# Kernel tuning notes

Hardware: AMD Instinct MI355X
Metric: run time of the kernel (lower is better)

The kernel has to match this reference:

```python
import jax, jax.numpy as jnp
import numpy as np

VOCAB, DIM, HID, OUT = 400000, 300, 32, 2
BATCH, SEQ = 16384, 50

def setup_inputs() -> dict:
    key = jax.random.key(0)
    k_tok, k_emb, k_vw, k_vb, k_ww, k_wb = jax.random.split(key, 6)
    tokens = jax.random.randint(k_tok, (BATCH, SEQ), 0, VOCAB, dtype=jnp.int32)
    emb = jax.random.normal(k_emb, (VOCAB, DIM), dtype=jnp.float32) * 0.02
    emb = emb.at[0].set(0.0)  # padding_idx=0 row conventionally zero
    V_w = jax.random.normal(k_vw, (HID, DIM), dtype=jnp.float32) * (1.0 / np.sqrt(DIM))
    V_b = jnp.zeros((HID,), dtype=jnp.float32)
    W_w = jax.random.normal(k_ww, (OUT, HID), dtype=jnp.float32) * (1.0 / np.sqrt(HID))
    W_b = jnp.zeros((OUT,), dtype=jnp.float32)
    return {"tokens": tokens, "emb": emb, "V_w": V_w, "V_b": V_b, "W_w": W_w, "W_b": W_b}

def reference(tokens, emb, V_w, V_b, W_w, W_b):
    # gather [B,S,D] then mean-pool over words -> [B,D] (DAN average)
    pooled = jnp.mean(emb[tokens], axis=1)
    h = jax.nn.relu(pooled @ V_w.T + V_b)          # [B,HID]
    logits = h @ W_w.T + W_b                        # [B,OUT]
    # original module uses LogSoftmax(dim=0): normalize over the batch axis
    return jax.nn.log_softmax(logits, axis=0)
```

## Files before the change

### kernel.cpp

```cpp
#include <hip/hip_runtime.h>

#define VOCAB 400000
#define DIM   300
#define HID   32
#define NOUT  2
#define BATCH 16384
#define SEQ   50

__global__ __launch_bounds__(256) void dan_main(
    const int*   __restrict__ tokens,
    const float* __restrict__ emb,
    const float* __restrict__ Vw,
    const float* __restrict__ Vb,
    const float* __restrict__ Ww,
    const float* __restrict__ Wb,
    float*       __restrict__ logits)
{
    const int wave = threadIdx.x >> 6;
    const int lane = threadIdx.x & 63;
    const int row  = blockIdx.x * 4 + wave;
    if (row >= BATCH) return;

    const int* toks = tokens + row * SEQ;

    const bool has1 = (lane < (DIM / 4 - 64));

    float4 acc0 = make_float4(0.f, 0.f, 0.f, 0.f);
    float4 acc1 = make_float4(0.f, 0.f, 0.f, 0.f);

    for (int s = 0; s < SEQ; ++s) {
        const int t = toks[s];
        const float4* e = (const float4*)(emb + (size_t)t * DIM);
        float4 v0 = e[lane];
        acc0.x += v0.x; acc0.y += v0.y; acc0.z += v0.z; acc0.w += v0.w;
        if (has1) {
            float4 v1 = e[64 + lane];
            acc1.x += v1.x; acc1.y += v1.y; acc1.z += v1.z; acc1.w += v1.w;
        }
    }
    const float inv = 1.0f / (float)SEQ;
    acc0.x *= inv; acc0.y *= inv; acc0.z *= inv; acc0.w *= inv;
    acc1.x *= inv; acc1.y *= inv; acc1.z *= inv; acc1.w *= inv;

    float hp[HID];
    #pragma unroll
    for (int k = 0; k < HID; ++k) {
        const float4* vr = (const float4*)(Vw + k * DIM);
        float4 w0 = vr[lane];
        float p = acc0.x * w0.x + acc0.y * w0.y + acc0.z * w0.z + acc0.w * w0.w;
        if (has1) {
            float4 w1 = vr[64 + lane];
            p += acc1.x * w1.x + acc1.y * w1.y + acc1.z * w1.z + acc1.w * w1.w;
        }
        hp[k] = p;
    }

    #pragma unroll
    for (int m = 1; m < 64; m <<= 1) {
        #pragma unroll
        for (int k = 0; k < HID; ++k)
            hp[k] += __shfl_xor(hp[k], m, 64);
    }

    float l0 = Wb[0], l1 = Wb[1];
    #pragma unroll
    for (int k = 0; k < HID; ++k) {
        float h = hp[k] + Vb[k];
        h = h > 0.f ? h : 0.f;
        l0 += h * Ww[k];
        l1 += h * Ww[HID + k];
    }
    if (lane == 0) {
        logits[row * 2 + 0] = l0;
        logits[row * 2 + 1] = l1;
    }
}

__global__ __launch_bounds__(1024) void dan_reduce(
    const float* __restrict__ logits, float* __restrict__ c)
{
    __shared__ float r0[1024];
    __shared__ float r1[1024];
    const int tid = threadIdx.x;

    float m0 = -INFINITY, m1 = -INFINITY;
    for (int b = tid; b < BATCH; b += 1024) {
        m0 = fmaxf(m0, logits[b * 2 + 0]);
        m1 = fmaxf(m1, logits[b * 2 + 1]);
    }
    r0[tid] = m0; r1[tid] = m1;
    __syncthreads();
    for (int s = 512; s > 0; s >>= 1) {
        if (tid < s) {
            r0[tid] = fmaxf(r0[tid], r0[tid + s]);
            r1[tid] = fmaxf(r1[tid], r1[tid + s]);
        }
        __syncthreads();
    }
    m0 = r0[0]; m1 = r1[0];
    __syncthreads();

    float s0 = 0.f, s1 = 0.f;
    for (int b = tid; b < BATCH; b += 1024) {
        s0 += __expf(logits[b * 2 + 0] - m0);
        s1 += __expf(logits[b * 2 + 1] - m1);
    }
    r0[tid] = s0; r1[tid] = s1;
    __syncthreads();
    for (int s = 512; s > 0; s >>= 1) {
        if (tid < s) {
            r0[tid] += r0[tid + s];
            r1[tid] += r1[tid + s];
        }
        __syncthreads();
    }
    if (tid == 0) {
        c[0] = m0 + __logf(r0[0]);
        c[1] = m1 + __logf(r1[0]);
    }
}

__global__ __launch_bounds__(256) void dan_final(
    const float* __restrict__ logits, const float* __restrict__ c,
    float* __restrict__ out)
{
    const int idx = blockIdx.x * blockDim.x + threadIdx.x;
    if (idx < BATCH * NOUT)
        out[idx] = logits[idx] - c[idx & 1];
}

extern "C" void kernel_launch(void* const* d_in, const int* in_sizes, int n_in,
                              void* d_out, int out_size, void* d_ws, size_t ws_size,
                              hipStream_t stream) {
    const int*   tokens = (const int*)  d_in[0];
    const float* emb    = (const float*)d_in[1];
    const float* Vw     = (const float*)d_in[2];
    const float* Vb     = (const float*)d_in[3];
    const float* Ww     = (const float*)d_in[4];
    const float* Wb     = (const float*)d_in[5];
    float* out    = (float*)d_out;
    float* logits = (float*)d_ws;
    float* c      = logits + BATCH * NOUT;

    dan_main  <<<BATCH / 4, 256, 0, stream>>>(tokens, emb, Vw, Vb, Ww, Wb, logits);
    dan_reduce<<<1, 1024, 0, stream>>>(logits, c);
    dan_final <<<(BATCH * NOUT + 255) / 256, 256, 0, stream>>>(logits, c, out);
}
```

Baseline: 770.3 us.

## Restructure hidden projection via shared memory and fuse final normalization kernel

The pooled vector is staged in shared memory, and each lane then computes one hidden unit's half dot product, replacing the 32-entry per-lane register array and its 6-stage shuffle reduction over 32 values. The launch bounds now request 8 blocks per CU and the gather loop is unrolled to raise occupancy and memory-level parallelism for the embedding gather. The final log-softmax subtraction is folded into the single-block reduce kernel, which removes one launch but makes one block write all outputs. Each lane now reads Vw rows directly from global or L2 memory at row-strided addresses, and a block-wide barrier is added.

```diff
diff --git a/kernel.cpp b/kernel.cpp
--- a/kernel.cpp
+++ b/kernel.cpp
@@ -7,7 +7,7 @@
 #define BATCH 16384
 #define SEQ   50
 
-__global__ __launch_bounds__(256) void dan_main(
+__global__ __launch_bounds__(256, 8) void dan_main(
     const int*   __restrict__ tokens,
     const float* __restrict__ emb,
     const float* __restrict__ Vw,
@@ -19,15 +19,14 @@
     const int wave = threadIdx.x >> 6;
     const int lane = threadIdx.x & 63;
     const int row  = blockIdx.x * 4 + wave;
-    if (row >= BATCH) return;
 
     const int* toks = tokens + row * SEQ;
-
     const bool has1 = (lane < (DIM / 4 - 64));
 
     float4 acc0 = make_float4(0.f, 0.f, 0.f, 0.f);
     float4 acc1 = make_float4(0.f, 0.f, 0.f, 0.f);
 
+    #pragma unroll 5
     for (int s = 0; s < SEQ; ++s) {
         const int t = toks[s];
         const float4* e = (const float4*)(emb + (size_t)t * DIM);
@@ -40,44 +39,51 @@
     }
     const float inv = 1.0f / (float)SEQ;
     acc0.x *= inv; acc0.y *= inv; acc0.z *= inv; acc0.w *= inv;
-    acc1.x *= inv; acc1.y *= inv; acc1.z *= inv; acc1.w *= inv;
 
-    float hp[HID];
+    __shared__ float pool[4][304];
+    *(float4*)&pool[wave][4 * lane] = acc0;
+    if (has1) {
+        acc1.x *= inv; acc1.y *= inv; acc1.z *= inv; acc1.w *= inv;
+        *(float4*)&pool[wave][256 + 4 * lane] = acc1;
+    }
+    __syncthreads();
+
+    const int k    = lane & 31;
+    const int half = lane >> 5;
+    const int base = half ? 152 : 0;
+    const float* __restrict__ vrow = Vw + k * DIM + base;
+    const float* pw = &pool[wave][base];
+
+    float p = 0.f;
     #pragma unroll
-    for (int k = 0; k < HID; ++k) {
-        const float4* vr = (const float4*)(Vw + k * DIM);
-        float4 w0 = vr[lane];
-        float p = acc0.x * w0.x + acc0.y * w0.y + acc0.z * w0.z + acc0.w * w0.w;
-        if (has1) {
-            float4 w1 = vr[64 + lane];
-            p += acc1.x * w1.x + acc1.y * w1.y + acc1.z * w1.z + acc1.w * w1.w;
-        }
-        hp[k] = p;
+    for (int i = 0; i < 37; ++i) {
+        float4 a = *(const float4*)(pw + 4 * i);
+        float4 w = *(const float4*)(vrow + 4 * i);
+        p += a.x * w.x + a.y * w.y + a.z * w.z + a.w * w.w;
     }
+    if (!half) {
+        float4 a = *(const float4*)(pw + 148);
+        float4 w = *(const float4*)(vrow + 148);
+        p += a.x * w.x + a.y * w.y + a.z * w.z + a.w * w.w;
+    }
+    p += __shfl_xor(p, 32, 64);
 
+    float hv = fmaxf(p + Vb[k], 0.f);
+    float g0 = hv * Ww[k];
+    float g1 = hv * Ww[HID + k];
     #pragma unroll
-    for (int m = 1; m < 64; m <<= 1) {
-        #pragma unroll
-        for (int k = 0; k < HID; ++k)
-            hp[k] += __shfl_xor(hp[k], m, 64);
-    }
-
-    float l0 = Wb[0], l1 = Wb[1];
-    #pragma unroll
-    for (int k = 0; k < HID; ++k) {
-        float h = hp[k] + Vb[k];
-        h = h > 0.f ? h : 0.f;
-        l0 += h * Ww[k];
-        l1 += h * Ww[HID + k];
+    for (int m = 1; m < 32; m <<= 1) {
+        g0 += __shfl_xor(g0, m, 64);
+        g1 += __shfl_xor(g1, m, 64);
     }
     if (lane == 0) {
-        logits[row * 2 + 0] = l0;
-        logits[row * 2 + 1] = l1;
+        logits[row * 2 + 0] = g0 + Wb[0];
+        logits[row * 2 + 1] = g1 + Wb[1];
     }
 }
 
-__global__ __launch_bounds__(1024) void dan_reduce(
-    const float* __restrict__ logits, float* __restrict__ c)
+__global__ __launch_bounds__(1024) void dan_reduce_final(
+    const float* __restrict__ logits, float* __restrict__ out)
 {
     __shared__ float r0[1024];
     __shared__ float r1[1024];
@@ -114,19 +120,11 @@
         }
         __syncthreads();
     }
-    if (tid == 0) {
-        c[0] = m0 + __logf(r0[0]);
-        c[1] = m1 + __logf(r1[0]);
+    const float c0 = m0 + __logf(r0[0]);
+    const float c1 = m1 + __logf(r1[0]);
+    for (int i = tid; i < BATCH * NOUT; i += 1024) {
+        out[i] = logits[i] - ((i & 1) ? c1 : c0);
     }
-}
-
-__global__ __launch_bounds__(256) void dan_final(
-    const float* __restrict__ logits, const float* __restrict__ c,
-    float* __restrict__ out)
-{
-    const int idx = blockIdx.x * blockDim.x + threadIdx.x;
-    if (idx < BATCH * NOUT)
-        out[idx] = logits[idx] - c[idx & 1];
 }
 
 extern "C" void kernel_launch(void* const* d_in, const int* in_sizes, int n_in,
@@ -140,9 +138,7 @@
     const float* Wb     = (const float*)d_in[5];
     float* out    = (float*)d_out;
     float* logits = (float*)d_ws;
-    float* c      = logits + BATCH * NOUT;
 
-    dan_main  <<<BATCH / 4, 256, 0, stream>>>(tokens, emb, Vw, Vb, Ww, Wb, logits);
-    dan_reduce<<<1, 1024, 0, stream>>>(logits, c);
-    dan_final <<<(BATCH * NOUT + 255) / 256, 256, 0, stream>>>(logits, c, out);
+    dan_main        <<<BATCH / 4, 256, 0, stream>>>(tokens, emb, Vw, Vb, Ww, Wb, logits);
+    dan_reduce_final<<<1, 1024, 0, stream>>>(logits, out);
 }
```

Result: faster. 742.8 us (-3.6%).
